# Performance work log

Measured on AMD Instinct MI355X. Metric: run time of the kernel, lower is better.

## Reference

```python
import jax, jax.numpy as jnp
import numpy as np

EPS = 1e-6


def setup_inputs() -> dict:
    key = jax.random.key(0)
    k = jax.random.split(key, 6)
    B, C_in, C_out, H, W, E = 32, 256, 256, 64, 64, 1024
    x = jax.random.normal(k[0], (B, C_in, H, W), dtype=jnp.float32)
    emb = jax.random.normal(k[1], (B, E), dtype=jnp.float32)
    # adaLN Linear(E -> 2*C_in). (Module zero-inits these; random here for coverage.)
    ada_w = jax.random.normal(k[2], (2 * C_in, E), dtype=jnp.float32) * 0.02
    ada_b = jax.random.normal(k[3], (2 * C_in,), dtype=jnp.float32) * 0.02
    # 1x1 Conv2d(C_in -> C_out) weight (C_out, C_in) and bias
    conv_w = jax.random.normal(k[4], (C_out, C_in), dtype=jnp.float32) * (1.0 / np.sqrt(C_in))
    conv_b = jax.random.normal(k[5], (C_out,), dtype=jnp.float32) * 0.02
    return {"x": x, "emb": emb, "ada_w": ada_w, "ada_b": ada_b,
            "conv_w": conv_w, "conv_b": conv_b}


def reference(x, emb, ada_w, ada_b, conv_w, conv_b):
    # adaLN modulation: SiLU(emb) @ W^T + b -> (B, 2C) -> shift, scale
    mod = jax.nn.silu(emb) @ ada_w.T + ada_b          # (B, 2C)
    shift, scale = jnp.split(mod, 2, axis=1)          # each (B, C)
    # RMSNorm over channel dim (no affine)
    rms = jax.lax.rsqrt(jnp.mean(x * x, axis=1, keepdims=True) + EPS)  # (B,1,H,W)
    xn = x * rms
    # modulate: x * (1 + scale) + shift, broadcast over H,W
    xm = xn * (1.0 + scale[:, :, None, None]) + shift[:, :, None, None]
    # 1x1 conv == channel GEMM
    y = jnp.einsum('bchw,oc->bohw', xm, conv_w) + conv_b[None, :, None, None]
    return jax.nn.selu(y)
```

## Files before the change

### kernel.cpp

```cpp
#include <hip/hip_runtime.h>
#include <hip/hip_bf16.h>

typedef __attribute__((ext_vector_type(4))) float f32x4;
typedef __attribute__((ext_vector_type(8))) short s16x8;
typedef __attribute__((ext_vector_type(4))) unsigned short u16x4;

__device__ __forceinline__ unsigned short f2bf(float f) {
  unsigned u = __builtin_bit_cast(unsigned, f);
  u += 0x7fffu + ((u >> 16) & 1u);
  return (unsigned short)(u >> 16);
}

__global__ __launch_bounds__(512) void k_mod(const float* __restrict__ emb,
                                             const float* __restrict__ ada_w,
                                             const float* __restrict__ ada_b,
                                             float* __restrict__ mod) {
  __shared__ __align__(16) float semb[32][1028];
  const int t = threadIdx.x;
  for (int i = t; i < 8192; i += 512) {
    f32x4 v = ((const f32x4*)emb)[i];
    f32x4 s;
#pragma unroll
    for (int j = 0; j < 4; ++j) s[j] = v[j] / (1.f + __expf(-v[j]));
    *(f32x4*)&semb[i >> 8][(i & 255) << 2] = s;
  }
  __syncthreads();
  const int jl = t >> 5, b = t & 31;
  const int j = blockIdx.x * 16 + jl;
  const f32x4* aw = (const f32x4*)(ada_w + (size_t)j * 1024);
  float acc = 0.f;
  for (int q = 0; q < 256; ++q) {
    f32x4 a = aw[q];
    f32x4 sv = *(const f32x4*)&semb[b][q * 4];
    acc += a[0] * sv[0] + a[1] * sv[1] + a[2] * sv[2] + a[3] * sv[3];
  }
  mod[b * 512 + j] = acc + ada_b[j];
}

__global__ __launch_bounds__(256) void k_prep(const float* __restrict__ mod,
                                              const float* __restrict__ conv_w,
                                              const float* __restrict__ conv_b,
                                              unsigned short* __restrict__ wp,
                                              float* __restrict__ dvec) {
  const int b = blockIdx.y;
  const int o = blockIdx.x * 4 + (threadIdx.x >> 6);
  const int l = threadIdx.x & 63;
  const float* sh = mod + b * 512;
  const float* sc = mod + b * 512 + 256;
  f32x4 cw = ((const f32x4*)(conv_w + (size_t)o * 256))[l];
  f32x4 s4 = ((const f32x4*)sc)[l];
  f32x4 h4 = ((const f32x4*)sh)[l];
  u16x4 wq;
#pragma unroll
  for (int j = 0; j < 4; ++j) wq[j] = f2bf(cw[j] * (1.f + s4[j]));
  *(u16x4*)(wp + (size_t)b * 65536 + o * 256 + 4 * l) = wq;
  float dd = cw[0] * h4[0] + cw[1] * h4[1] + cw[2] * h4[2] + cw[3] * h4[3];
#pragma unroll
  for (int off = 32; off; off >>= 1) dd += __shfl_down(dd, off);
  if (l == 0) dvec[b * 256 + o] = dd + conv_b[o];
}

__device__ __forceinline__ void stage_a(const unsigned short* __restrict__ Wb, int k0,
                                        unsigned char* as_buf, int w, int lane) {
#pragma unroll
  for (int i = 0; i < 2; ++i) {
    int row = (w * 2 + i) * 16 + (lane >> 2);
    const unsigned short* gp = Wb + row * 256 + k0 + (lane & 3) * 8;
    void* lp = as_buf + (w * 2 + i) * 1024;
    __builtin_amdgcn_global_load_lds((const __attribute__((address_space(1))) void*)gp,
                                     (__attribute__((address_space(3))) void*)lp, 16, 0, 0);
  }
}

__global__ __launch_bounds__(512, 4) void k_main(const float* __restrict__ x,
                                                 const unsigned short* __restrict__ wp,
                                                 const float* __restrict__ dvec,
                                                 float* __restrict__ out) {
  constexpr int HW = 4096;
  __shared__ __align__(16) unsigned char lds_as[2 * 16384];
  __shared__ __align__(16) unsigned short lds_bt[64 * 256];
  __shared__ float lds_part[32 * 64];
  __shared__ float lds_rms[64];
  __shared__ float lds_d[256];

  const int t = threadIdx.x;
  const int b = blockIdx.y;
  const int s0 = blockIdx.x * 64;
  const int w = t >> 6, lane = t & 63;
  const int wr = w >> 1, wc = w & 1;
  const int lr = lane & 15, g = lane >> 4;

  const unsigned short* Wb = wp + (size_t)b * 65536;

  stage_a(Wb, 0, lds_as, w, lane);
  if (t < 256) lds_d[t] = dvec[b * 256 + t];

  const float* xb = x + (size_t)b * (256 * HW) + s0;
  const int sq = t & 15, cg = t >> 4;
  f32x4 sacc = {0.f, 0.f, 0.f, 0.f};
#pragma unroll
  for (int it = 0; it < 8; ++it) {
    int c = cg + 32 * it;
    f32x4 v = *(const f32x4*)(xb + (size_t)c * HW + 4 * sq);
    sacc += v * v;
#pragma unroll
    for (int r = 0; r < 4; ++r) {
      int s = 4 * sq + r;
      lds_bt[s * 256 + (c ^ (((s >> 1) & 7) << 3))] = f2bf(v[r]);
    }
  }
  *(f32x4*)(lds_part + cg * 64 + 4 * sq) = sacc;
  __syncthreads();
  if (t < 64) {
    float sum = 0.f;
#pragma unroll 8
    for (int q = 0; q < 32; ++q) sum += lds_part[q * 64 + t];
    lds_rms[t] = rsqrtf(sum * (1.0f / 256.0f) + 1e-6f);
  }

  f32x4 acc[4][2] = {};
  const int sA = 32 * wc + lr;
  const int sB = sA + 16;

  for (int kk = 0; kk < 8; ++kk) {
    const int cur = kk & 1;
    __syncthreads();
    if (kk < 7) stage_a(Wb, (kk + 1) * 32, lds_as + (cur ^ 1) * 16384, w, lane);

    s16x8 af[4];
#pragma unroll
    for (int m = 0; m < 4; ++m)
      af[m] = *(const s16x8*)(lds_as + cur * 16384 + (64 * wr + 16 * m + lr) * 64 + g * 16);

    const int c0 = kk * 32 + g * 8;
    s16x8 b0 = *(const s16x8*)&lds_bt[sA * 256 + (c0 ^ (((sA >> 1) & 7) << 3))];
    s16x8 b1 = *(const s16x8*)&lds_bt[sB * 256 + (c0 ^ (((sB >> 1) & 7) << 3))];

#pragma unroll
    for (int m = 0; m < 4; ++m) {
      acc[m][0] = __builtin_amdgcn_mfma_f32_16x16x32_bf16(af[m], b0, acc[m][0], 0, 0, 0);
      acc[m][1] = __builtin_amdgcn_mfma_f32_16x16x32_bf16(af[m], b1, acc[m][1], 0, 0, 0);
    }
  }

  float* ob = out + (size_t)b * (256 * HW) + s0;
#pragma unroll
  for (int m = 0; m < 4; ++m) {
    const int o0 = 64 * wr + 16 * m + 4 * g;
#pragma unroll
    for (int n = 0; n < 2; ++n) {
      const int s = 32 * wc + 16 * n + lr;
      const float rr = lds_rms[s];
#pragma unroll
      for (int r = 0; r < 4; ++r) {
        float v = rr * acc[m][n][r] + lds_d[o0 + r];
        float res = v > 0.f ? 1.0507009873554805f * v
                            : 1.7580993408473766f * expm1f(v);
        ob[(size_t)(o0 + r) * HW + s] = res;
      }
    }
  }
}

extern "C" void kernel_launch(void* const* d_in, const int* in_sizes, int n_in,
                              void* d_out, int out_size, void* d_ws, size_t ws_size,
                              hipStream_t stream) {
  const float* x      = (const float*)d_in[0];
  const float* emb    = (const float*)d_in[1];
  const float* ada_w  = (const float*)d_in[2];
  const float* ada_b  = (const float*)d_in[3];
  const float* conv_w = (const float*)d_in[4];
  const float* conv_b = (const float*)d_in[5];
  float* out = (float*)d_out;

  float* mod  = (float*)d_ws;
  float* dvec = mod + 32 * 512;
  unsigned short* wp = (unsigned short*)(dvec + 32 * 256);

  k_mod<<<dim3(32), 512, 0, stream>>>(emb, ada_w, ada_b, mod);
  k_prep<<<dim3(64, 32), 256, 0, stream>>>(mod, conv_w, conv_b, wp, dvec);
  k_main<<<dim3(64, 32), 512, 0, stream>>>(x, wp, dvec, out);
}
```

Measured before the change: 102.3 us.

## Pre-swizzle weights into MFMA fragment layout and load A directly from global

```diff
diff --git a/kernel.cpp b/kernel.cpp
--- a/kernel.cpp
+++ b/kernel.cpp
@@ -53,23 +53,13 @@
   u16x4 wq;
 #pragma unroll
   for (int j = 0; j < 4; ++j) wq[j] = f2bf(cw[j] * (1.f + s4[j]));
-  *(u16x4*)(wp + (size_t)b * 65536 + o * 256 + 4 * l) = wq;
+  const int wr = o >> 6, m = (o >> 4) & 3, lr = o & 15;
+  const int kk = l >> 3, g = (l >> 1) & 3, jb = 4 * (l & 1);
+  *(u16x4*)(wp + (size_t)b * 65536 + (((wr * 4 + m) * 8 + kk) * 512 + g * 128 + lr * 8 + jb)) = wq;
   float dd = cw[0] * h4[0] + cw[1] * h4[1] + cw[2] * h4[2] + cw[3] * h4[3];
 #pragma unroll
   for (int off = 32; off; off >>= 1) dd += __shfl_down(dd, off);
   if (l == 0) dvec[b * 256 + o] = dd + conv_b[o];
-}
-
-__device__ __forceinline__ void stage_a(const unsigned short* __restrict__ Wb, int k0,
-                                        unsigned char* as_buf, int w, int lane) {
-#pragma unroll
-  for (int i = 0; i < 2; ++i) {
-    int row = (w * 2 + i) * 16 + (lane >> 2);
-    const unsigned short* gp = Wb + row * 256 + k0 + (lane & 3) * 8;
-    void* lp = as_buf + (w * 2 + i) * 1024;
-    __builtin_amdgcn_global_load_lds((const __attribute__((address_space(1))) void*)gp,
-                                     (__attribute__((address_space(3))) void*)lp, 16, 0, 0);
-  }
 }
 
 __global__ __launch_bounds__(512, 4) void k_main(const float* __restrict__ x,
@@ -77,9 +67,8 @@
                                                  const float* __restrict__ dvec,
                                                  float* __restrict__ out) {
   constexpr int HW = 4096;
-  __shared__ __align__(16) unsigned char lds_as[2 * 16384];
   __shared__ __align__(16) unsigned short lds_bt[64 * 256];
-  __shared__ float lds_part[32 * 64];
+  __shared__ float lds_part[8][64];
   __shared__ float lds_rms[64];
   __shared__ float lds_d[256];
 
@@ -90,9 +79,8 @@
   const int wr = w >> 1, wc = w & 1;
   const int lr = lane & 15, g = lane >> 4;
 
-  const unsigned short* Wb = wp + (size_t)b * 65536;
+  const unsigned short* A2 = wp + (size_t)b * 65536;
 
-  stage_a(Wb, 0, lds_as, w, lane);
   if (t < 256) lds_d[t] = dvec[b * 256 + t];
 
   const float* xb = x + (size_t)b * (256 * HW) + s0;
@@ -109,28 +97,31 @@
       lds_bt[s * 256 + (c ^ (((s >> 1) & 7) << 3))] = f2bf(v[r]);
     }
   }
-  *(f32x4*)(lds_part + cg * 64 + 4 * sq) = sacc;
+#pragma unroll
+  for (int off = 16; off <= 32; off <<= 1) {
+#pragma unroll
+    for (int j = 0; j < 4; ++j) sacc[j] += __shfl_xor(sacc[j], off);
+  }
+  if (lane < 16) *(f32x4*)&lds_part[w][4 * sq] = sacc;
   __syncthreads();
   if (t < 64) {
     float sum = 0.f;
-#pragma unroll 8
-    for (int q = 0; q < 32; ++q) sum += lds_part[q * 64 + t];
+#pragma unroll
+    for (int q = 0; q < 8; ++q) sum += lds_part[q][t];
     lds_rms[t] = rsqrtf(sum * (1.0f / 256.0f) + 1e-6f);
   }
+  __syncthreads();
 
   f32x4 acc[4][2] = {};
   const int sA = 32 * wc + lr;
   const int sB = sA + 16;
 
+#pragma unroll
   for (int kk = 0; kk < 8; ++kk) {
-    const int cur = kk & 1;
-    __syncthreads();
-    if (kk < 7) stage_a(Wb, (kk + 1) * 32, lds_as + (cur ^ 1) * 16384, w, lane);
-
     s16x8 af[4];
 #pragma unroll
     for (int m = 0; m < 4; ++m)
-      af[m] = *(const s16x8*)(lds_as + cur * 16384 + (64 * wr + 16 * m + lr) * 64 + g * 16);
+      af[m] = *(const s16x8*)(A2 + (((wr * 4 + m) * 8 + kk) * 512 + lane * 8));
 
     const int c0 = kk * 32 + g * 8;
     s16x8 b0 = *(const s16x8*)&lds_bt[sA * 256 + (c0 ^ (((sA >> 1) & 7) << 3))];
```

Measured after the change: 101.0 us. About the same (-1.2%).
